# Kernel tuning notes

Measured on AMD Instinct MI355X. Metric: run time of the kernel, lower is better.

## Reference

```python
import jax, jax.numpy as jnp
import numpy as np

B, S, D = 2, 4096, 1024
H, HD = 16, 64
CF = 0.5
K = int(S * CF)          # top_k tokens routed through the block
HIDDEN = 4 * D
EPS = 1e-5
SCALE = 1.0 / float(np.sqrt(HD))


def rmsnorm(x, w):
    return x * jax.lax.rsqrt(jnp.mean(x * x, axis=-1, keepdims=True) + EPS) * w


def rope(x, cos, sin):
    # x: [B,K,H,HD]; cos/sin: [K, HD//2]
    x1, x2 = x[..., ::2], x[..., 1::2]
    c = cos[None, :, None, :]
    s = sin[None, :, None, :]
    r1 = x1 * c - x2 * s
    r2 = x1 * s + x2 * c
    return jnp.stack([r1, r2], axis=-1).reshape(x.shape)


def block(x, mask, cos, sin, attn_norm, wq, wk, wv, wo, ffn_norm, w1, w2, w3):
    # Llama-style decoder block on the routed subset x: [B,K,D]
    b, k, _ = x.shape
    xn = rmsnorm(x, attn_norm)
    q = (xn @ wq).reshape(b, k, H, HD)
    kk = (xn @ wk).reshape(b, k, H, HD)
    v = (xn @ wv).reshape(b, k, H, HD)
    q = rope(q, cos, sin)
    kk = rope(kk, cos, sin)
    scores = jnp.einsum('bqhd,bkhd->bhqk', q, kk) * SCALE
    scores = jnp.where(mask[None, None], scores, jnp.finfo(scores.dtype).min)
    attn = jax.nn.softmax(scores, axis=-1)
    o = jnp.einsum('bhqk,bkhd->bqhd', attn, v).reshape(b, k, D)
    h = x + o @ wo
    hn = rmsnorm(h, ffn_norm)
    return h + (jax.nn.silu(hn @ w1) * (hn @ w3)) @ w2


def setup_inputs() -> dict:
    key = jax.random.key(0)
    ks = jax.random.split(key, 10)
    sc = 0.02
    inv = 1.0 / (10000.0 ** (np.arange(0, HD, 2, dtype=np.float32) / HD))
    ang = np.outer(np.arange(K, dtype=np.float32), inv)  # [K, HD//2]
    return {
        'x': jax.random.normal(ks[0], (B, S, D), jnp.float32),
        'mask': jnp.tril(jnp.ones((K, K), dtype=bool)),
        'freqs_cos': jnp.asarray(np.cos(ang)),
        'freqs_sin': jnp.asarray(np.sin(ang)),
        'w_router': jax.random.normal(ks[1], (D, 1), jnp.float32) * sc,
        'attn_norm': jnp.ones((D,), jnp.float32),
        'wq': jax.random.normal(ks[2], (D, D), jnp.float32) * sc,
        'wk': jax.random.normal(ks[3], (D, D), jnp.float32) * sc,
        'wv': jax.random.normal(ks[4], (D, D), jnp.float32) * sc,
        'wo': jax.random.normal(ks[5], (D, D), jnp.float32) * sc,
        'ffn_norm': jnp.ones((D,), jnp.float32),
        'w1': jax.random.normal(ks[6], (D, HIDDEN), jnp.float32) * sc,
        'w2': jax.random.normal(ks[7], (HIDDEN, D), jnp.float32) * sc,
        'w3': jax.random.normal(ks[8], (D, HIDDEN), jnp.float32) * sc,
    }


def reference(x, mask, freqs_cos, freqs_sin, w_router, attn_norm, wq, wk, wv, wo, ffn_norm, w1, w2, w3):
    b = x.shape[0]
    router_logits = (x @ w_router)[..., 0]            # [B,S]
    vals, idx = jax.lax.top_k(router_logits, K)       # [B,K]
    order = jnp.argsort(idx, axis=1)                  # torch.sort of token_index
    sel = jnp.take_along_axis(idx, order, axis=1)     # sorted selected positions
    token_w = jax.nn.softmax(vals, axis=1)            # softmax over topk weights
    r_weights = jnp.take_along_axis(token_w, order, axis=1)  # [B,K]
    filtered_x = jnp.take_along_axis(x, sel[:, :, None], axis=1)  # [B,K,D]
    x_out = block(filtered_x, mask, freqs_cos, freqs_sin, attn_norm,
                  wq, wk, wv, wo, ffn_norm, w1, w2, w3)
    xw_out = r_weights[:, :, None] * x_out
    # scatter_add back into the residual stream
    out = x.at[jnp.arange(b)[:, None], sel, :].add(xw_out)
    return out
```

## Files before the change

kernel.cpp:

```cpp
#include <hip/hip_runtime.h>
#include <cstdint>
#include <cstddef>

typedef unsigned short u16;
typedef __bf16 bf16x8 __attribute__((ext_vector_type(8)));
typedef short s16x4 __attribute__((ext_vector_type(4)));
typedef float f32x4 __attribute__((ext_vector_type(4)));

#define SCALE_Q_LOG2E 0.18033688011112042f

static __device__ __forceinline__ float b2f(u16 u){ return __uint_as_float(((unsigned)u)<<16); }
static __device__ __forceinline__ u16 f2b(float f){
  unsigned u = __float_as_uint(f);
  return (u16)((u + 0x7fffu + ((u>>16)&1u)) >> 16);
}
static __device__ __forceinline__ void gload_lds16(const void* g, void* l){
  auto gp = reinterpret_cast<__attribute__((address_space(1))) uint32_t*>(reinterpret_cast<uintptr_t>(g));
  auto lp = reinterpret_cast<__attribute__((address_space(3))) uint32_t*>(reinterpret_cast<uintptr_t>(l));
  __builtin_amdgcn_global_load_lds(gp, lp, 16, 0, 0);
}
static __device__ __forceinline__ f32x4 mfma16bf(s16x4 a, s16x4 b, f32x4 c){
#if __has_builtin(__builtin_amdgcn_mfma_f32_16x16x16bf16_1k)
  return __builtin_amdgcn_mfma_f32_16x16x16bf16_1k(a, b, c, 0, 0, 0);
#else
  f32x4 d = c;
  asm volatile("v_mfma_f32_16x16x16_bf16 %0, %1, %2, %0" : "+v"(d) : "v"(a), "v"(b));
  return d;
#endif
}

__global__ __launch_bounds__(256) void transpose_f2b(const float* __restrict__ in, u16* __restrict__ out,
                                                     int R, int C, int rowmap){
  __shared__ float tile[32][33];
  int tx = threadIdx.x, ty = threadIdx.y;
  int c0 = blockIdx.x*32, r0 = blockIdx.y*32;
  #pragma unroll
  for (int i=0;i<4;i++) tile[ty+i*8][tx] = in[(size_t)(r0+ty+i*8)*C + c0+tx];
  __syncthreads();
  #pragma unroll
  for (int i=0;i<4;i++){
    int c = c0+ty+i*8;
    int orow = c;
    if (rowmap==1) orow = (c>>4)*32 + (c&15);
    else if (rowmap==2) orow = (c>>4)*32 + 16 + (c&15);
    out[(size_t)orow*R + r0+tx] = f2b(tile[tx][ty+i*8]);
  }
}

__global__ __launch_bounds__(256) void transpose_bf16(const u16* __restrict__ in, u16* __restrict__ out,
                                                      int R, int C){
  __shared__ u16 tile[32][33];
  size_t zoff = (size_t)blockIdx.z * R * C;
  const u16* ip = in + zoff;
  u16* op = out + zoff;
  int tx = threadIdx.x, ty = threadIdx.y;
  int c0 = blockIdx.x*32, r0 = blockIdx.y*32;
  #pragma unroll
  for (int i=0;i<4;i++) tile[ty+i*8][tx] = ip[(size_t)(r0+ty+i*8)*C + c0+tx];
  __syncthreads();
  #pragma unroll
  for (int i=0;i<4;i++) op[(size_t)(c0+ty+i*8)*R + r0+tx] = tile[tx][ty+i*8];
}

__global__ __launch_bounds__(256) void router_kernel(const float* __restrict__ x, const float* __restrict__ wr,
                                                     float* __restrict__ logits){
  int row = blockIdx.x*4 + (threadIdx.x>>6);
  int l = threadIdx.x & 63;
  const float4* xr = (const float4*)(x + (size_t)row*1024) + l;
  const float4* wp = (const float4*)wr + l;
  float acc = 0.f;
  #pragma unroll
  for (int c=0;c<4;c++){
    float4 xv = xr[c*64];
    float4 wv = wp[c*64];
    acc += xv.x*wv.x + xv.y*wv.y + xv.z*wv.z + xv.w*wv.w;
  }
  #pragma unroll
  for (int m=1;m<64;m<<=1) acc += __shfl_xor(acc, m, 64);
  if (l==0) logits[row] = acc;
}

static __device__ __forceinline__ unsigned mapkey(float f){
  unsigned u = __float_as_uint(f);
  return (u & 0x80000000u) ? ~u : (u | 0x80000000u);
}
static __device__ unsigned blk_scan_excl(unsigned cnt, unsigned* swav){
  int t = threadIdx.x; int l = t&63, w = t>>6;
  unsigned v = cnt;
  #pragma unroll
  for (int off=1; off<64; off<<=1){
    unsigned n = __shfl_up(v, off, 64);
    if (l >= off) v += n;
  }
  __syncthreads();
  if (l==63) swav[w] = v;
  __syncthreads();
  if (t==0){ unsigned c=0; for (int i=0;i<16;i++){ unsigned tmp=swav[i]; swav[i]=c; c+=tmp; } }
  __syncthreads();
  return swav[w] + v - cnt;
}
__global__ __launch_bounds__(1024) void topk_kernel(const float* __restrict__ logits,
        int* __restrict__ sel, float* __restrict__ rw, int* __restrict__ inv){
  int b = blockIdx.x, t = threadIdx.x;
  int l = t&63, w = t>>6;
  __shared__ float vals[4096];
  __shared__ unsigned hist[256];
  __shared__ unsigned swav[16];
  __shared__ float fwav[16];
  __shared__ unsigned sh_prefix, sh_remaining;
  const float* lgp = logits + b*4096;
  for (int i=t;i<4096;i+=1024) vals[i]=lgp[i];
  if (t==0){ sh_prefix=0u; sh_remaining=2048u; }
  __syncthreads();
  for (int level=0; level<4; level++){
    int shift = 24 - level*8;
    if (t<256) hist[t]=0u;
    __syncthreads();
    unsigned pfx = sh_prefix;
    for (int i=t;i<4096;i+=1024){
      unsigned key = mapkey(vals[i]);
      if (level==0 || (key >> (shift+8)) == pfx)
        atomicAdd(&hist[(key>>shift)&255u], 1u);
    }
    __syncthreads();
    if (t==0){
      unsigned rem = sh_remaining, cum=0u; unsigned bsel=0u;
      for (int bin=255; bin>=0; bin--){
        unsigned hc = hist[bin];
        if (cum + hc >= rem){ bsel=(unsigned)bin; break; }
        cum += hc;
      }
      sh_remaining = rem - cum;
      sh_prefix = (pfx<<8) | bsel;
    }
    __syncthreads();
  }
  unsigned T = sh_prefix;
  unsigned req = sh_remaining;
  int i0 = t*4;
  unsigned gt_[4], eq_[4], fl_[4]; float v_[4];
  #pragma unroll
  for (int j=0;j<4;j++){
    v_[j] = vals[i0+j];
    unsigned key = mapkey(v_[j]);
    gt_[j] = key > T ? 1u:0u;
    eq_[j] = key == T ? 1u:0u;
  }
  unsigned eqbase = blk_scan_excl(eq_[0]+eq_[1]+eq_[2]+eq_[3], swav);
  unsigned er = eqbase;
  #pragma unroll
  for (int j=0;j<4;j++){ fl_[j] = gt_[j] | (eq_[j] & (er < req ? 1u:0u)); er += eq_[j]; }
  unsigned pbase = blk_scan_excl(fl_[0]+fl_[1]+fl_[2]+fl_[3], swav);
  unsigned p = pbase;
  #pragma unroll
  for (int j=0;j<4;j++){
    int i = i0+j;
    if (fl_[j]){ sel[b*2048+(int)p]=i; inv[b*4096+i]=(int)p; p++; }
    else inv[b*4096+i] = -1;
  }
  float mx = fmaxf(fmaxf(v_[0],v_[1]), fmaxf(v_[2],v_[3]));
  #pragma unroll
  for (int m=1;m<64;m<<=1) mx = fmaxf(mx, __shfl_xor(mx,m,64));
  __syncthreads();
  if (l==0) fwav[w]=mx;
  __syncthreads();
  if (t==0){ float g=fwav[0]; for(int i=1;i<16;i++) g=fmaxf(g,fwav[i]); fwav[0]=g; }
  __syncthreads();
  float gm = fwav[0];
  float zz = 0.f;
  #pragma unroll
  for (int j=0;j<4;j++) if (fl_[j]) zz += expf(v_[j]-gm);
  #pragma unroll
  for (int m=1;m<64;m<<=1) zz += __shfl_xor(zz,m,64);
  __syncthreads();
  if (l==0) fwav[w]=zz;
  __syncthreads();
  if (t==0){ float s=0.f; for(int i=0;i<16;i++) s+=fwav[i]; fwav[0]=s; }
  __syncthreads();
  float Z = fwav[0];
  unsigned p2 = pbase;
  #pragma unroll
  for (int j=0;j<4;j++) if (fl_[j]){ rw[b*2048+(int)p2] = expf(v_[j]-gm)/Z; p2++; }
}

__global__ __launch_bounds__(256) void rmsnorm_kernel(const float* __restrict__ xin,
        const float* __restrict__ gamma, const int* __restrict__ sel,
        u16* __restrict__ xn){
  int r = blockIdx.x;
  int src = r;
  if (sel) src = (r>>11)*4096 + sel[r];
  const float* row = xin + (size_t)src*1024;
  int t = threadIdx.x, l = t&63, w = t>>6;
  int d0 = t*4;
  float4 xv = *(const float4*)(row + d0);
  float ss = xv.x*xv.x + xv.y*xv.y + xv.z*xv.z + xv.w*xv.w;
  #pragma unroll
  for (int m=1;m<64;m<<=1) ss += __shfl_xor(ss,m,64);
  __shared__ float red[4];
  if (l==0) red[w]=ss;
  __syncthreads();
  float tot = red[0]+red[1]+red[2]+red[3];
  float rms = rsqrtf(tot*(1.f/1024.f) + 1e-5f);
  float4 gv = *(const float4*)(gamma + d0);
  u16 o0=f2b(xv.x*rms*gv.x), o1=f2b(xv.y*rms*gv.y), o2=f2b(xv.z*rms*gv.z), o3=f2b(xv.w*rms*gv.w);
  uint2 ov; ov.x = (unsigned)o0 | ((unsigned)o1<<16); ov.y = (unsigned)o2 | ((unsigned)o3<<16);
  *(uint2*)(xn + (size_t)r*1024 + d0) = ov;
}

template<int BN, int BK, typename OT>
__global__ __launch_bounds__(256,2) void gemm_bt(const u16* __restrict__ A, const u16* __restrict__ Bt,
        OT* __restrict__ C, const float* __restrict__ resid, const int* __restrict__ sel,
        int M, int N, int Kd){
  __shared__ u16 As[128*BK];
  __shared__ u16 Bs[BN*BK];
  constexpr int NF = BN/32;
  constexpr int KK = BK/32;
  int t = threadIdx.x, w = t>>6, l = t&63, lg = l>>4, ln = l&15;
  int m0 = blockIdx.y*128, n0 = blockIdx.x*BN;
  int wm = (w&1)*64, wn = (w>>1)*(BN/2);
  f32x4 acc[4][NF] = {};
  for (int k0=0; k0<Kd; k0+=BK){
    __syncthreads();
    #pragma unroll
    for (int c=0;c<128*BK*2/4096;c++){
      int off = t*16 + c*4096;
      int row = off/(BK*2), ku = (off%(BK*2))>>1;
      gload_lds16(A + (size_t)(m0+row)*Kd + k0 + ku, &As[c*2048 + w*512]);
    }
    #pragma unroll
    for (int c=0;c<BN*BK*2/4096;c++){
      int off = t*16 + c*4096;
      int row = off/(BK*2), ku = (off%(BK*2))>>1;
      gload_lds16(Bt + (size_t)(n0+row)*Kd + k0 + ku, &Bs[c*2048 + w*512]);
    }
    __syncthreads();
    #pragma unroll
    for (int kk=0;kk<KK;kk++){
      bf16x8 af[4], bfv[NF];
      #pragma unroll
      for (int i=0;i<4;i++)  af[i]  = *(const bf16x8*)&As[(wm+i*16+ln)*BK + kk*32 + lg*8];
      #pragma unroll
      for (int i=0;i<NF;i++) bfv[i] = *(const bf16x8*)&Bs[(wn+i*16+ln)*BK + kk*32 + lg*8];
      #pragma unroll
      for (int mi=0;mi<4;mi++)
        #pragma unroll
        for (int ni=0;ni<NF;ni++)
          acc[mi][ni] = __builtin_amdgcn_mfma_f32_16x16x32_bf16(af[mi], bfv[ni], acc[mi][ni], 0,0,0);
    }
  }
  #pragma unroll
  for (int mi=0;mi<4;mi++){
    #pragma unroll
    for (int ni=0;ni<NF;ni++){
      #pragma unroll
      for (int r=0;r<4;r++){
        int row = m0+wm+mi*16+lg*4+r;
        int col = n0+wn+ni*16+ln;
        float v = acc[mi][ni][r];
        if (resid){
          size_t rrow = sel ? ((size_t)(row>>11)*4096 + sel[row]) : (size_t)row;
          v += resid[rrow*N + col];
        }
        if constexpr (sizeof(OT)==2) C[(size_t)row*N + col] = f2b(v);
        else                          C[(size_t)row*N + col] = v;
      }
    }
  }
}

__global__ __launch_bounds__(256,2) void gemm13(const u16* __restrict__ A, const u16* __restrict__ Bt,
        u16* __restrict__ g, int Kd){
  __shared__ u16 As[128*32];
  __shared__ u16 Bs[128*32];
  int t = threadIdx.x, w = t>>6, l = t&63, lg = l>>4, ln = l&15;
  int m0 = blockIdx.y*128, n0 = blockIdx.x*128;
  int wm = (w&1)*64, wn = (w>>1)*64;
  f32x4 acc[4][4] = {};
  for (int k0=0; k0<Kd; k0+=32){
    __syncthreads();
    #pragma unroll
    for (int c=0;c<2;c++){
      int off = t*16 + c*4096;
      int row = off>>6, ku = (off&63)>>1;
      gload_lds16(A  + (size_t)(m0+row)*Kd + k0 + ku, &As[c*2048 + w*512]);
      gload_lds16(Bt + (size_t)(n0+row)*Kd + k0 + ku, &Bs[c*2048 + w*512]);
    }
    __syncthreads();
    bf16x8 af[4], bfv[4];
    #pragma unroll
    for (int i=0;i<4;i++){
      af[i]  = *(const bf16x8*)&As[(wm+i*16+ln)*32 + lg*8];
      bfv[i] = *(const bf16x8*)&Bs[(wn+i*16+ln)*32 + lg*8];
    }
    #pragma unroll
    for (int mi=0;mi<4;mi++)
      #pragma unroll
      for (int ni=0;ni<4;ni++)
        acc[mi][ni] = __builtin_amdgcn_mfma_f32_16x16x32_bf16(af[mi], bfv[ni], acc[mi][ni], 0,0,0);
  }
  int gbase = (n0+wn)>>1;
  #pragma unroll
  for (int mi=0;mi<4;mi++){
    #pragma unroll
    for (int p=0;p<2;p++){
      #pragma unroll
      for (int r=0;r<4;r++){
        int row = m0+wm+mi*16+lg*4+r;
        int col = gbase + p*16 + ln;
        float a1 = acc[mi][2*p][r], a3 = acc[mi][2*p+1][r];
        float s1 = a1 / (1.f + __expf(-a1));
        g[(size_t)row*4096 + col] = f2b(s1*a3);
      }
    }
  }
}

__global__ __launch_bounds__(256) void rope_kernel(const u16* __restrict__ QKV,
        const float* __restrict__ fcos, const float* __restrict__ fsin,
        u16* __restrict__ q_r, u16* __restrict__ k_r, u16* __restrict__ v_r){
  int row = blockIdx.x;
  int tok = row & 2047;
  int t = threadIdx.x;
  int d0 = t*4;
  int h = d0 >> 6, wd = d0 & 63, i0 = wd >> 1;
  const u16* base = QKV + (size_t)row*3072;
  size_t ob = (((size_t)(row>>11)*16 + h)*2048 + (size_t)tok)*64 + wd;
  float c0 = fcos[tok*32+i0],   s0 = fsin[tok*32+i0];
  float c1 = fcos[tok*32+i0+1], s1 = fsin[tok*32+i0+1];
  const u16* qp = base + d0;
  float x0=b2f(qp[0]), x1=b2f(qp[1]), x2=b2f(qp[2]), x3=b2f(qp[3]);
  q_r[ob]   = f2b((x0*c0-x1*s0)*SCALE_Q_LOG2E);
  q_r[ob+1] = f2b((x0*s0+x1*c0)*SCALE_Q_LOG2E);
  q_r[ob+2] = f2b((x2*c1-x3*s1)*SCALE_Q_LOG2E);
  q_r[ob+3] = f2b((x2*s1+x3*c1)*SCALE_Q_LOG2E);
  const u16* kp = base + 1024 + d0;
  x0=b2f(kp[0]); x1=b2f(kp[1]); x2=b2f(kp[2]); x3=b2f(kp[3]);
  k_r[ob]   = f2b(x0*c0-x1*s0);
  k_r[ob+1] = f2b(x0*s0+x1*c0);
  k_r[ob+2] = f2b(x2*c1-x3*s1);
  k_r[ob+3] = f2b(x2*s1+x3*c1);
  const u16* vp = base + 2048 + d0;
  v_r[ob]=vp[0]; v_r[ob+1]=vp[1]; v_r[ob+2]=vp[2]; v_r[ob+3]=vp[3];
}

__global__ __launch_bounds__(256,2) void flash_kernel(const u16* __restrict__ q_r,
        const u16* __restrict__ k_r, const u16* __restrict__ v_t, u16* __restrict__ o){
  const int S = 2048;
  int pr = blockIdx.x, bh = blockIdx.y;
  int b = bh>>4, h = bh&15;
  int t = threadIdx.x, w = t>>6, l = t&63, lg = l>>4, ln = l&15;
  __shared__ u16 Ks[2][64*72];
  __shared__ u16 Vs[2][64*72];
  const u16* qb = q_r + (size_t)bh*S*64;
  const u16* kb = k_r + (size_t)bh*S*64;
  const u16* vb = v_t + (size_t)bh*64*S;
  int rr = t>>2, p16 = (t&3)*16;
  #pragma unroll
  for (int ti=0; ti<2; ti++){
    int qt = ti ? (31-pr) : pr;
    int q0 = qt*64;
    int q = q0 + w*16 + ln;
    bf16x8 qf0 = *(const bf16x8*)(qb + (size_t)q*64 + lg*8);
    bf16x8 qf1 = *(const bf16x8*)(qb + (size_t)q*64 + 32 + lg*8);
    f32x4 oaccT[4] = {};
    float mi = -1e30f, li = 0.f;
    __syncthreads();
    {
      *(bf16x8*)&Ks[0][rr*72+p16]   = *(const bf16x8*)(kb + (size_t)rr*64 + p16);
      *(bf16x8*)&Ks[0][rr*72+p16+8] = *(const bf16x8*)(kb + (size_t)rr*64 + p16 + 8);
      *(bf16x8*)&Vs[0][rr*72+p16]   = *(const bf16x8*)(vb + (size_t)rr*S + p16);
      *(bf16x8*)&Vs[0][rr*72+p16+8] = *(const bf16x8*)(vb + (size_t)rr*S + p16 + 8);
    }
    __syncthreads();
    for (int kv=0; kv<=qt; kv++){
      int cur = kv&1;
      int k0 = kv*64;
      bool hasnext = kv < qt;
      bf16x8 nk0, nk1, nv0, nv1;
      if (hasnext){
        int kn = k0 + 64;
        nk0 = *(const bf16x8*)(kb + (size_t)(kn+rr)*64 + p16);
        nk1 = *(const bf16x8*)(kb + (size_t)(kn+rr)*64 + p16 + 8);
        nv0 = *(const bf16x8*)(vb + (size_t)rr*S + kn + p16);
        nv1 = *(const bf16x8*)(vb + (size_t)rr*S + kn + p16 + 8);
      }
      f32x4 sv[4];
      #pragma unroll
      for (int ni=0;ni<4;ni++){
        bf16x8 kf0 = *(const bf16x8*)&Ks[cur][(ni*16+ln)*72 + lg*8];
        bf16x8 kf1 = *(const bf16x8*)&Ks[cur][(ni*16+ln)*72 + 32 + lg*8];
        f32x4 z = {};
        z = __builtin_amdgcn_mfma_f32_16x16x32_bf16(kf0, qf0, z, 0,0,0);
        z = __builtin_amdgcn_mfma_f32_16x16x32_bf16(kf1, qf1, z, 0,0,0);
        sv[ni] = z;
      }
      bool diag = (kv==qt);
      float rm = -1e30f;
      if (diag){
        #pragma unroll
        for (int ni=0;ni<4;ni++)
          #pragma unroll
          for (int r=0;r<4;r++){
            float xs = sv[ni][r];
            if (k0+ni*16+lg*4+r > q) xs = -1e30f;
            sv[ni][r] = xs;
            rm = fmaxf(rm, xs);
          }
      } else {
        #pragma unroll
        for (int ni=0;ni<4;ni++)
          #pragma unroll
          for (int r=0;r<4;r++) rm = fmaxf(rm, sv[ni][r]);
      }
      rm = fmaxf(rm, __shfl_xor(rm, 16, 64));
      rm = fmaxf(rm, __shfl_xor(rm, 32, 64));
      float mn = fmaxf(mi, rm);
      float alpha = exp2f(mi - mn);
      float ls = 0.f;
      s16x4 pf[4];
      #pragma unroll
      for (int ni=0;ni<4;ni++){
        float p0 = exp2f(sv[ni][0]-mn);
        float p1 = exp2f(sv[ni][1]-mn);
        float p2 = exp2f(sv[ni][2]-mn);
        float p3 = exp2f(sv[ni][3]-mn);
        ls += (p0+p1)+(p2+p3);
        s16x4 pp;
        pp[0]=(short)f2b(p0); pp[1]=(short)f2b(p1); pp[2]=(short)f2b(p2); pp[3]=(short)f2b(p3);
        pf[ni]=pp;
      }
      ls += __shfl_xor(ls, 16, 64);
      ls += __shfl_xor(ls, 32, 64);
      li = li*alpha + ls;
      mi = mn;
      #pragma unroll
      for (int dt=0; dt<4; dt++){
        f32x4 oo = oaccT[dt];
        oo[0]*=alpha; oo[1]*=alpha; oo[2]*=alpha; oo[3]*=alpha;
        #pragma unroll
        for (int ni=0;ni<4;ni++){
          s16x4 vf = *(const s16x4*)&Vs[cur][(dt*16+ln)*72 + ni*16 + lg*4];
          oo = mfma16bf(vf, pf[ni], oo);
        }
        oaccT[dt] = oo;
      }
      if (hasnext){
        int nb = cur^1;
        *(bf16x8*)&Ks[nb][rr*72+p16]   = nk0;
        *(bf16x8*)&Ks[nb][rr*72+p16+8] = nk1;
        *(bf16x8*)&Vs[nb][rr*72+p16]   = nv0;
        *(bf16x8*)&Vs[nb][rr*72+p16+8] = nv1;
      }
      __syncthreads();
    }
    {
      int tok = q0 + w*16 + ln;
      u16* ob = o + ((size_t)(b*S+tok))*1024 + h*64 + lg*4;
      #pragma unroll
      for (int dt=0; dt<4; dt++){
        u16 a0=f2b(oaccT[dt][0]/li), a1=f2b(oaccT[dt][1]/li);
        u16 a2=f2b(oaccT[dt][2]/li), a3=f2b(oaccT[dt][3]/li);
        uint2 pv; pv.x = (unsigned)a0 | ((unsigned)a1<<16); pv.y = (unsigned)a2 | ((unsigned)a3<<16);
        *(uint2*)(ob + dt*16) = pv;
      }
    }
  }
}

__global__ __launch_bounds__(256) void final_kernel(const float* __restrict__ x, const float* __restrict__ h,
        const u16* __restrict__ y, const int* __restrict__ inv, const float* __restrict__ rw,
        float* __restrict__ out){
  int row = blockIdx.x;
  int b = row>>12;
  int t = threadIdx.x, d0 = t*4;
  float4 xv = *(const float4*)(x + (size_t)row*1024 + d0);
  float4* op = (float4*)(out + (size_t)row*1024 + d0);
  int j = inv[row];
  if (j < 0){ *op = xv; return; }
  int fr = b*2048 + j;
  float wgt = rw[fr];
  float4 hv = *(const float4*)(h + (size_t)fr*1024 + d0);
  uint2 yv = *(const uint2*)(y + (size_t)fr*1024 + d0);
  float y0=b2f((u16)(yv.x&0xffffu)), y1=b2f((u16)(yv.x>>16)), y2=b2f((u16)(yv.y&0xffffu)), y3=b2f((u16)(yv.y>>16));
  float4 ov;
  ov.x = xv.x + wgt*(hv.x + y0);
  ov.y = xv.y + wgt*(hv.y + y1);
  ov.z = xv.z + wgt*(hv.z + y2);
  ov.w = xv.w + wgt*(hv.w + y3);
  *op = ov;
}

extern "C" void kernel_launch(void* const* d_in, const int* in_sizes, int n_in,
                              void* d_out, int out_size, void* d_ws, size_t ws_size,
                              hipStream_t stream) {
  (void)in_sizes; (void)n_in; (void)out_size; (void)ws_size;
  const float* x     = (const float*)d_in[0];
  const float* fcos  = (const float*)d_in[2];
  const float* fsin  = (const float*)d_in[3];
  const float* wr    = (const float*)d_in[4];
  const float* anorm = (const float*)d_in[5];
  const float* wq    = (const float*)d_in[6];
  const float* wk    = (const float*)d_in[7];
  const float* wv    = (const float*)d_in[8];
  const float* wo    = (const float*)d_in[9];
  const float* fnorm = (const float*)d_in[10];
  const float* w1    = (const float*)d_in[11];
  const float* w2    = (const float*)d_in[12];
  const float* w3    = (const float*)d_in[13];
  float* out = (float*)d_out;

  char* W = (char*)d_ws;
  const size_t MB = 1024*1024;
  u16* WqkvT = (u16*)(W + 0);
  u16* WoT   = (u16*)(W + 6*MB);
  u16* W13T  = (u16*)(W + 8*MB);
  u16* W2T   = (u16*)(W + 24*MB);
  u16* xn    = (u16*)(W + 32*MB);
  u16* QKV   = (u16*)(W + 40*MB);
  u16* q_r   = (u16*)(W + 64*MB);
  u16* k_r   = (u16*)(W + 72*MB);
  u16* v_r   = (u16*)(W + 80*MB);
  u16* v_t   = (u16*)(W + 88*MB);
  u16* attno = (u16*)(W + 96*MB);
  float* hbuf= (float*)(W + 104*MB);
  u16* hn    = (u16*)(W + 120*MB);
  u16* g     = (u16*)(W + 128*MB);
  u16* ybuf  = (u16*)(W + 32*MB);
  float* logits = (float*)(W + 160*MB);
  int*   sel    = (int*)(W + 160*MB + 64*1024);
  float* rw     = (float*)(W + 160*MB + 96*1024);
  int*   inv    = (int*)(W + 160*MB + 128*1024);

  dim3 tb(32,8);
  transpose_f2b<<<dim3(32,32,1),  tb, 0, stream>>>(wq, WqkvT,                1024, 1024, 0);
  transpose_f2b<<<dim3(32,32,1),  tb, 0, stream>>>(wk, WqkvT + 1024*1024,    1024, 1024, 0);
  transpose_f2b<<<dim3(32,32,1),  tb, 0, stream>>>(wv, WqkvT + 2*1024*1024,  1024, 1024, 0);
  transpose_f2b<<<dim3(32,32,1),  tb, 0, stream>>>(wo, WoT,                  1024, 1024, 0);
  transpose_f2b<<<dim3(128,32,1), tb, 0, stream>>>(w1, W13T,                 1024, 4096, 1);
  transpose_f2b<<<dim3(128,32,1), tb, 0, stream>>>(w3, W13T,                 1024, 4096, 2);
  transpose_f2b<<<dim3(32,128,1), tb, 0, stream>>>(w2, W2T,                  4096, 1024, 0);

  router_kernel<<<2048, 256, 0, stream>>>(x, wr, logits);
  topk_kernel<<<2, 1024, 0, stream>>>(logits, sel, rw, inv);
  rmsnorm_kernel<<<4096, 256, 0, stream>>>(x, anorm, sel, xn);
  gemm_bt<128,32,u16><<<dim3(24,32), 256, 0, stream>>>(xn, WqkvT, QKV, nullptr, nullptr, 4096, 3072, 1024);
  rope_kernel<<<4096, 256, 0, stream>>>(QKV, fcos, fsin, q_r, k_r, v_r);
  transpose_bf16<<<dim3(2,64,32), tb, 0, stream>>>(v_r, v_t, 2048, 64);
  flash_kernel<<<dim3(16,32), 256, 0, stream>>>(q_r, k_r, v_t, attno);
  gemm_bt<64,32,float><<<dim3(16,32), 256, 0, stream>>>(attno, WoT, hbuf, x, sel, 4096, 1024, 1024);
  rmsnorm_kernel<<<4096, 256, 0, stream>>>(hbuf, fnorm, nullptr, hn);
  gemm13<<<dim3(64,32), 256, 0, stream>>>(hn, W13T, g, 1024);
  gemm_bt<64,64,u16><<<dim3(16,32), 256, 0, stream>>>(g, W2T, ybuf, nullptr, nullptr, 4096, 1024, 4096);
  final_kernel<<<8192, 256, 0, stream>>>(x, hbuf, ybuf, inv, rw, out);
}
```

Before: 526.5 us.

## Swizzle GEMM LDS tiles, deepen K tiles, fuse weight prep, share KV across query tiles

Merges the seven weight transpose launches into one prep_weights kernel. Adds an XOR swizzle to the GEMM LDS layout to cut bank conflicts, and raises the K tile to 64 for the QKV, Wo and W1/W3 GEMMs so each barrier covers more MFMAs. The flash kernel now handles its two query tiles (low and high) in a single pass over K/V, so shared tiles are loaded once and used by both. This adds register pressure (two accumulator sets) and more LDS per block, which may lower occupancy.

```diff
diff --git a/kernel.cpp b/kernel.cpp
--- a/kernel.cpp
+++ b/kernel.cpp
@@ -29,11 +29,32 @@
 #endif
 }
 
-__global__ __launch_bounds__(256) void transpose_f2b(const float* __restrict__ in, u16* __restrict__ out,
-                                                     int R, int C, int rowmap){
+__global__ __launch_bounds__(256) void prep_weights(
+    const float* __restrict__ wq, const float* __restrict__ wk,
+    const float* __restrict__ wv, const float* __restrict__ wo,
+    const float* __restrict__ w1, const float* __restrict__ w3,
+    const float* __restrict__ w2,
+    u16* __restrict__ WqkvT, u16* __restrict__ WoT,
+    u16* __restrict__ W13T, u16* __restrict__ W2T){
   __shared__ float tile[32][33];
-  int tx = threadIdx.x, ty = threadIdx.y;
-  int c0 = blockIdx.x*32, r0 = blockIdx.y*32;
+  int bx = blockIdx.x;
+  const float* in; u16* out; int R, C, rowmap, tcol, trow;
+  if (bx < 4096){
+    int wsel = bx>>10, tid = bx&1023;
+    in = (wsel==0)?wq:(wsel==1)?wk:(wsel==2)?wv:wo;
+    out = (wsel<3) ? (WqkvT + (size_t)wsel*1024*1024) : WoT;
+    R=1024; C=1024; rowmap=0; tcol=tid&31; trow=tid>>5;
+  } else if (bx < 12288){
+    int wsel=(bx-4096)>>12, tid=(bx-4096)&4095;
+    in = wsel ? w3 : w1; out = W13T; R=1024; C=4096; rowmap=1+wsel;
+    tcol=tid&127; trow=tid>>7;
+  } else {
+    int tid = bx-12288;
+    in = w2; out = W2T; R=4096; C=1024; rowmap=0;
+    tcol=tid&31; trow=tid>>5;
+  }
+  int t=threadIdx.x, tx=t&31, ty=t>>5;
+  int c0=tcol*32, r0=trow*32;
   #pragma unroll
   for (int i=0;i<4;i++) tile[ty+i*8][tx] = in[(size_t)(r0+ty+i*8)*C + c0+tx];
   __syncthreads();
@@ -205,6 +226,12 @@
   u16 o0=f2b(xv.x*rms*gv.x), o1=f2b(xv.y*rms*gv.y), o2=f2b(xv.z*rms*gv.z), o3=f2b(xv.w*rms*gv.w);
   uint2 ov; ov.x = (unsigned)o0 | ((unsigned)o1<<16); ov.y = (unsigned)o2 | ((unsigned)o3<<16);
   *(uint2*)(xn + (size_t)r*1024 + d0) = ov;
+}
+
+template<int BK>
+static __device__ __forceinline__ int swz(int row, int blk){
+  if constexpr (BK==64) return blk ^ (row&7);
+  else                  return blk ^ ((row>>1)&3);
 }
 
 template<int BN, int BK, typename OT>
@@ -224,23 +251,29 @@
     #pragma unroll
     for (int c=0;c<128*BK*2/4096;c++){
       int off = t*16 + c*4096;
-      int row = off/(BK*2), ku = (off%(BK*2))>>1;
-      gload_lds16(A + (size_t)(m0+row)*Kd + k0 + ku, &As[c*2048 + w*512]);
+      int row = off/(BK*2), pb = (off%(BK*2))>>4;
+      gload_lds16(A + (size_t)(m0+row)*Kd + k0 + swz<BK>(row,pb)*8, &As[c*2048 + w*512]);
     }
     #pragma unroll
     for (int c=0;c<BN*BK*2/4096;c++){
       int off = t*16 + c*4096;
-      int row = off/(BK*2), ku = (off%(BK*2))>>1;
-      gload_lds16(Bt + (size_t)(n0+row)*Kd + k0 + ku, &Bs[c*2048 + w*512]);
+      int row = off/(BK*2), pb = (off%(BK*2))>>4;
+      gload_lds16(Bt + (size_t)(n0+row)*Kd + k0 + swz<BK>(row,pb)*8, &Bs[c*2048 + w*512]);
     }
     __syncthreads();
     #pragma unroll
     for (int kk=0;kk<KK;kk++){
       bf16x8 af[4], bfv[NF];
       #pragma unroll
-      for (int i=0;i<4;i++)  af[i]  = *(const bf16x8*)&As[(wm+i*16+ln)*BK + kk*32 + lg*8];
-      #pragma unroll
-      for (int i=0;i<NF;i++) bfv[i] = *(const bf16x8*)&Bs[(wn+i*16+ln)*BK + kk*32 + lg*8];
+      for (int i=0;i<4;i++){
+        int r = wm+i*16+ln;
+        af[i] = *(const bf16x8*)&As[r*BK + swz<BK>(r, kk*4+lg)*8];
+      }
+      #pragma unroll
+      for (int i=0;i<NF;i++){
+        int r = wn+i*16+ln;
+        bfv[i] = *(const bf16x8*)&Bs[r*BK + swz<BK>(r, kk*4+lg)*8];
+      }
       #pragma unroll
       for (int mi=0;mi<4;mi++)
         #pragma unroll
@@ -270,33 +303,38 @@
 
 __global__ __launch_bounds__(256,2) void gemm13(const u16* __restrict__ A, const u16* __restrict__ Bt,
         u16* __restrict__ g, int Kd){
-  __shared__ u16 As[128*32];
-  __shared__ u16 Bs[128*32];
+  constexpr int BK = 64;
+  __shared__ u16 As[128*BK];
+  __shared__ u16 Bs[128*BK];
   int t = threadIdx.x, w = t>>6, l = t&63, lg = l>>4, ln = l&15;
   int m0 = blockIdx.y*128, n0 = blockIdx.x*128;
   int wm = (w&1)*64, wn = (w>>1)*64;
   f32x4 acc[4][4] = {};
-  for (int k0=0; k0<Kd; k0+=32){
-    __syncthreads();
-    #pragma unroll
-    for (int c=0;c<2;c++){
+  for (int k0=0; k0<Kd; k0+=BK){
+    __syncthreads();
+    #pragma unroll
+    for (int c=0;c<4;c++){
       int off = t*16 + c*4096;
-      int row = off>>6, ku = (off&63)>>1;
-      gload_lds16(A  + (size_t)(m0+row)*Kd + k0 + ku, &As[c*2048 + w*512]);
-      gload_lds16(Bt + (size_t)(n0+row)*Kd + k0 + ku, &Bs[c*2048 + w*512]);
-    }
-    __syncthreads();
-    bf16x8 af[4], bfv[4];
-    #pragma unroll
-    for (int i=0;i<4;i++){
-      af[i]  = *(const bf16x8*)&As[(wm+i*16+ln)*32 + lg*8];
-      bfv[i] = *(const bf16x8*)&Bs[(wn+i*16+ln)*32 + lg*8];
-    }
-    #pragma unroll
-    for (int mi=0;mi<4;mi++)
-      #pragma unroll
-      for (int ni=0;ni<4;ni++)
-        acc[mi][ni] = __builtin_amdgcn_mfma_f32_16x16x32_bf16(af[mi], bfv[ni], acc[mi][ni], 0,0,0);
+      int row = off/(BK*2), pb = (off%(BK*2))>>4;
+      gload_lds16(A  + (size_t)(m0+row)*Kd + k0 + swz<BK>(row,pb)*8, &As[c*2048 + w*512]);
+      gload_lds16(Bt + (size_t)(n0+row)*Kd + k0 + swz<BK>(row,pb)*8, &Bs[c*2048 + w*512]);
+    }
+    __syncthreads();
+    #pragma unroll
+    for (int kk=0;kk<2;kk++){
+      bf16x8 af[4], bfv[4];
+      #pragma unroll
+      for (int i=0;i<4;i++){
+        int ra = wm+i*16+ln, rb = wn+i*16+ln;
+        af[i]  = *(const bf16x8*)&As[ra*BK + swz<BK>(ra, kk*4+lg)*8];
+        bfv[i] = *(const bf16x8*)&Bs[rb*BK + swz<BK>(rb, kk*4+lg)*8];
+      }
+      #pragma unroll
+      for (int mi=0;mi<4;mi++)
+        #pragma unroll
+        for (int ni=0;ni<4;ni++)
+          acc[mi][ni] = __builtin_amdgcn_mfma_f32_16x16x32_bf16(af[mi], bfv[ni], acc[mi][ni], 0,0,0);
+    }
   }
   int gbase = (n0+wn)>>1;
   #pragma unroll
@@ -343,6 +381,71 @@
   v_r[ob]=vp[0]; v_r[ob+1]=vp[1]; v_r[ob+2]=vp[2]; v_r[ob+3]=vp[3];
 }
 
+static __device__ __forceinline__ void flash_tile(
+    const u16* __restrict__ Ksb, const u16* __restrict__ Vsb,
+    bf16x8 qf0, bf16x8 qf1, int k0, int q, bool diag,
+    int lg, int ln, float& mi, float& li, f32x4* oaccT){
+  f32x4 sv[4];
+  #pragma unroll
+  for (int ni=0;ni<4;ni++){
+    bf16x8 kf0 = *(const bf16x8*)&Ksb[(ni*16+ln)*72 + lg*8];
+    bf16x8 kf1 = *(const bf16x8*)&Ksb[(ni*16+ln)*72 + 32 + lg*8];
+    f32x4 z = {};
+    z = __builtin_amdgcn_mfma_f32_16x16x32_bf16(kf0, qf0, z, 0,0,0);
+    z = __builtin_amdgcn_mfma_f32_16x16x32_bf16(kf1, qf1, z, 0,0,0);
+    sv[ni] = z;
+  }
+  float rm = -1e30f;
+  if (diag){
+    #pragma unroll
+    for (int ni=0;ni<4;ni++)
+      #pragma unroll
+      for (int r=0;r<4;r++){
+        float xs = sv[ni][r];
+        if (k0+ni*16+lg*4+r > q) xs = -1e30f;
+        sv[ni][r] = xs;
+        rm = fmaxf(rm, xs);
+      }
+  } else {
+    #pragma unroll
+    for (int ni=0;ni<4;ni++)
+      #pragma unroll
+      for (int r=0;r<4;r++) rm = fmaxf(rm, sv[ni][r]);
+  }
+  rm = fmaxf(rm, __shfl_xor(rm, 16, 64));
+  rm = fmaxf(rm, __shfl_xor(rm, 32, 64));
+  float mn = fmaxf(mi, rm);
+  float alpha = exp2f(mi - mn);
+  float ls = 0.f;
+  s16x4 pf[4];
+  #pragma unroll
+  for (int ni=0;ni<4;ni++){
+    float p0 = exp2f(sv[ni][0]-mn);
+    float p1 = exp2f(sv[ni][1]-mn);
+    float p2 = exp2f(sv[ni][2]-mn);
+    float p3 = exp2f(sv[ni][3]-mn);
+    ls += (p0+p1)+(p2+p3);
+    s16x4 pp;
+    pp[0]=(short)f2b(p0); pp[1]=(short)f2b(p1); pp[2]=(short)f2b(p2); pp[3]=(short)f2b(p3);
+    pf[ni]=pp;
+  }
+  ls += __shfl_xor(ls, 16, 64);
+  ls += __shfl_xor(ls, 32, 64);
+  li = li*alpha + ls;
+  mi = mn;
+  #pragma unroll
+  for (int dt=0; dt<4; dt++){
+    f32x4 oo = oaccT[dt];
+    oo[0]*=alpha; oo[1]*=alpha; oo[2]*=alpha; oo[3]*=alpha;
+    #pragma unroll
+    for (int ni=0;ni<4;ni++){
+      s16x4 vf = *(const s16x4*)&Vsb[(dt*16+ln)*72 + ni*16 + lg*4];
+      oo = mfma16bf(vf, pf[ni], oo);
+    }
+    oaccT[dt] = oo;
+  }
+}
+
 __global__ __launch_bounds__(256,2) void flash_kernel(const u16* __restrict__ q_r,
         const u16* __restrict__ k_r, const u16* __restrict__ v_t, u16* __restrict__ o){
   const int S = 2048;
@@ -355,114 +458,64 @@
   const u16* kb = k_r + (size_t)bh*S*64;
   const u16* vb = v_t + (size_t)bh*64*S;
   int rr = t>>2, p16 = (t&3)*16;
-  #pragma unroll
-  for (int ti=0; ti<2; ti++){
-    int qt = ti ? (31-pr) : pr;
-    int q0 = qt*64;
-    int q = q0 + w*16 + ln;
-    bf16x8 qf0 = *(const bf16x8*)(qb + (size_t)q*64 + lg*8);
-    bf16x8 qf1 = *(const bf16x8*)(qb + (size_t)q*64 + 32 + lg*8);
-    f32x4 oaccT[4] = {};
-    float mi = -1e30f, li = 0.f;
-    __syncthreads();
-    {
-      *(bf16x8*)&Ks[0][rr*72+p16]   = *(const bf16x8*)(kb + (size_t)rr*64 + p16);
-      *(bf16x8*)&Ks[0][rr*72+p16+8] = *(const bf16x8*)(kb + (size_t)rr*64 + p16 + 8);
-      *(bf16x8*)&Vs[0][rr*72+p16]   = *(const bf16x8*)(vb + (size_t)rr*S + p16);
-      *(bf16x8*)&Vs[0][rr*72+p16+8] = *(const bf16x8*)(vb + (size_t)rr*S + p16 + 8);
-    }
-    __syncthreads();
-    for (int kv=0; kv<=qt; kv++){
-      int cur = kv&1;
-      int k0 = kv*64;
-      bool hasnext = kv < qt;
-      bf16x8 nk0, nk1, nv0, nv1;
-      if (hasnext){
-        int kn = k0 + 64;
-        nk0 = *(const bf16x8*)(kb + (size_t)(kn+rr)*64 + p16);
-        nk1 = *(const bf16x8*)(kb + (size_t)(kn+rr)*64 + p16 + 8);
-        nv0 = *(const bf16x8*)(vb + (size_t)rr*S + kn + p16);
-        nv1 = *(const bf16x8*)(vb + (size_t)rr*S + kn + p16 + 8);
-      }
-      f32x4 sv[4];
-      #pragma unroll
-      for (int ni=0;ni<4;ni++){
-        bf16x8 kf0 = *(const bf16x8*)&Ks[cur][(ni*16+ln)*72 + lg*8];
-        bf16x8 kf1 = *(const bf16x8*)&Ks[cur][(ni*16+ln)*72 + 32 + lg*8];
-        f32x4 z = {};
-        z = __builtin_amdgcn_mfma_f32_16x16x32_bf16(kf0, qf0, z, 0,0,0);
-        z = __builtin_amdgcn_mfma_f32_16x16x32_bf16(kf1, qf1, z, 0,0,0);
-        sv[ni] = z;
-      }
-      bool diag = (kv==qt);
-      float rm = -1e30f;
-      if (diag){
-        #pragma unroll
-        for (int ni=0;ni<4;ni++)
-          #pragma unroll
-          for (int r=0;r<4;r++){
-            float xs = sv[ni][r];
-            if (k0+ni*16+lg*4+r > q) xs = -1e30f;
-            sv[ni][r] = xs;
-            rm = fmaxf(rm, xs);
-          }
-      } else {
-        #pragma unroll
-        for (int ni=0;ni<4;ni++)
-          #pragma unroll
-          for (int r=0;r<4;r++) rm = fmaxf(rm, sv[ni][r]);
-      }
-      rm = fmaxf(rm, __shfl_xor(rm, 16, 64));
-      rm = fmaxf(rm, __shfl_xor(rm, 32, 64));
-      float mn = fmaxf(mi, rm);
-      float alpha = exp2f(mi - mn);
-      float ls = 0.f;
-      s16x4 pf[4];
-      #pragma unroll
-      for (int ni=0;ni<4;ni++){
-        float p0 = exp2f(sv[ni][0]-mn);
-        float p1 = exp2f(sv[ni][1]-mn);
-        float p2 = exp2f(sv[ni][2]-mn);
-        float p3 = exp2f(sv[ni][3]-mn);
-        ls += (p0+p1)+(p2+p3);
-        s16x4 pp;
-        pp[0]=(short)f2b(p0); pp[1]=(short)f2b(p1); pp[2]=(short)f2b(p2); pp[3]=(short)f2b(p3);
-        pf[ni]=pp;
-      }
-      ls += __shfl_xor(ls, 16, 64);
-      ls += __shfl_xor(ls, 32, 64);
-      li = li*alpha + ls;
-      mi = mn;
-      #pragma unroll
-      for (int dt=0; dt<4; dt++){
-        f32x4 oo = oaccT[dt];
-        oo[0]*=alpha; oo[1]*=alpha; oo[2]*=alpha; oo[3]*=alpha;
-        #pragma unroll
-        for (int ni=0;ni<4;ni++){
-          s16x4 vf = *(const s16x4*)&Vs[cur][(dt*16+ln)*72 + ni*16 + lg*4];
-          oo = mfma16bf(vf, pf[ni], oo);
-        }
-        oaccT[dt] = oo;
-      }
-      if (hasnext){
-        int nb = cur^1;
-        *(bf16x8*)&Ks[nb][rr*72+p16]   = nk0;
-        *(bf16x8*)&Ks[nb][rr*72+p16+8] = nk1;
-        *(bf16x8*)&Vs[nb][rr*72+p16]   = nv0;
-        *(bf16x8*)&Vs[nb][rr*72+p16+8] = nv1;
-      }
-      __syncthreads();
-    }
-    {
-      int tok = q0 + w*16 + ln;
-      u16* ob = o + ((size_t)(b*S+tok))*1024 + h*64 + lg*4;
-      #pragma unroll
-      for (int dt=0; dt<4; dt++){
-        u16 a0=f2b(oaccT[dt][0]/li), a1=f2b(oaccT[dt][1]/li);
-        u16 a2=f2b(oaccT[dt][2]/li), a3=f2b(oaccT[dt][3]/li);
-        uint2 pv; pv.x = (unsigned)a0 | ((unsigned)a1<<16); pv.y = (unsigned)a2 | ((unsigned)a3<<16);
-        *(uint2*)(ob + dt*16) = pv;
-      }
+  int qlo = pr, qhi = 31-pr;
+  int qAr = qlo*64 + w*16 + ln;
+  int qBr = qhi*64 + w*16 + ln;
+  bf16x8 qA0 = *(const bf16x8*)(qb + (size_t)qAr*64 + lg*8);
+  bf16x8 qA1 = *(const bf16x8*)(qb + (size_t)qAr*64 + 32 + lg*8);
+  bf16x8 qB0 = *(const bf16x8*)(qb + (size_t)qBr*64 + lg*8);
+  bf16x8 qB1 = *(const bf16x8*)(qb + (size_t)qBr*64 + 32 + lg*8);
+  f32x4 oA[4] = {}, oB[4] = {};
+  float miA=-1e30f, liA=0.f, miB=-1e30f, liB=0.f;
+  {
+    *(bf16x8*)&Ks[0][rr*72+p16]   = *(const bf16x8*)(kb + (size_t)rr*64 + p16);
+    *(bf16x8*)&Ks[0][rr*72+p16+8] = *(const bf16x8*)(kb + (size_t)rr*64 + p16 + 8);
+    *(bf16x8*)&Vs[0][rr*72+p16]   = *(const bf16x8*)(vb + (size_t)rr*S + p16);
+    *(bf16x8*)&Vs[0][rr*72+p16+8] = *(const bf16x8*)(vb + (size_t)rr*S + p16 + 8);
+  }
+  __syncthreads();
+  for (int kv=0; kv<=qhi; kv++){
+    int cur = kv&1;
+    int k0 = kv*64;
+    bool hasnext = kv < qhi;
+    bf16x8 nk0, nk1, nv0, nv1;
+    if (hasnext){
+      int kn = k0 + 64;
+      nk0 = *(const bf16x8*)(kb + (size_t)(kn+rr)*64 + p16);
+      nk1 = *(const bf16x8*)(kb + (size_t)(kn+rr)*64 + p16 + 8);
+      nv0 = *(const bf16x8*)(vb + (size_t)rr*S + kn + p16);
+      nv1 = *(const bf16x8*)(vb + (size_t)rr*S + kn + p16 + 8);
+    }
+    if (kv <= qlo)
+      flash_tile(Ks[cur], Vs[cur], qA0, qA1, k0, qAr, kv==qlo, lg, ln, miA, liA, oA);
+    flash_tile(Ks[cur], Vs[cur], qB0, qB1, k0, qBr, kv==qhi, lg, ln, miB, liB, oB);
+    if (hasnext){
+      int nb = cur^1;
+      *(bf16x8*)&Ks[nb][rr*72+p16]   = nk0;
+      *(bf16x8*)&Ks[nb][rr*72+p16+8] = nk1;
+      *(bf16x8*)&Vs[nb][rr*72+p16]   = nv0;
+      *(bf16x8*)&Vs[nb][rr*72+p16+8] = nv1;
+    }
+    __syncthreads();
+  }
+  {
+    u16* ob = o + ((size_t)(b*S+qAr))*1024 + h*64 + lg*4;
+    #pragma unroll
+    for (int dt=0; dt<4; dt++){
+      u16 a0=f2b(oA[dt][0]/liA), a1=f2b(oA[dt][1]/liA);
+      u16 a2=f2b(oA[dt][2]/liA), a3=f2b(oA[dt][3]/liA);
+      uint2 pv; pv.x = (unsigned)a0 | ((unsigned)a1<<16); pv.y = (unsigned)a2 | ((unsigned)a3<<16);
+      *(uint2*)(ob + dt*16) = pv;
+    }
+  }
+  {
+    u16* ob = o + ((size_t)(b*S+qBr))*1024 + h*64 + lg*4;
+    #pragma unroll
+    for (int dt=0; dt<4; dt++){
+      u16 a0=f2b(oB[dt][0]/liB), a1=f2b(oB[dt][1]/liB);
+      u16 a2=f2b(oB[dt][2]/liB), a3=f2b(oB[dt][3]/liB);
+      uint2 pv; pv.x = (unsigned)a0 | ((unsigned)a1<<16); pv.y = (unsigned)a2 | ((unsigned)a3<<16);
+      *(uint2*)(ob + dt*16) = pv;
     }
   }
 }
@@ -531,23 +584,15 @@
   float* rw     = (float*)(W + 160*MB + 96*1024);
   int*   inv    = (int*)(W + 160*MB + 128*1024);
 
-  dim3 tb(32,8);
-  transpose_f2b<<<dim3(32,32,1),  tb, 0, stream>>>(wq, WqkvT,                1024, 1024, 0);
-  transpose_f2b<<<dim3(32,32,1),  tb, 0, stream>>>(wk, WqkvT + 1024*1024,    1024, 1024, 0);
-  transpose_f2b<<<dim3(32,32,1),  tb, 0, stream>>>(wv, WqkvT + 2*1024*1024,  1024, 1024, 0);
-  transpose_f2b<<<dim3(32,32,1),  tb, 0, stream>>>(wo, WoT,                  1024, 1024, 0);
-  transpose_f2b<<<dim3(128,32,1), tb, 0, stream>>>(w1, W13T,                 1024, 4096, 1);
-  transpose_f2b<<<dim3(128,32,1), tb, 0, stream>>>(w3, W13T,                 1024, 4096, 2);
-  transpose_f2b<<<dim3(32,128,1), tb, 0, stream>>>(w2, W2T,                  4096, 1024, 0);
-
+  prep_weights<<<16384, 256, 0, stream>>>(wq, wk, wv, wo, w1, w3, w2, WqkvT, WoT, W13T, W2T);
   router_kernel<<<2048, 256, 0, stream>>>(x, wr, logits);
   topk_kernel<<<2, 1024, 0, stream>>>(logits, sel, rw, inv);
   rmsnorm_kernel<<<4096, 256, 0, stream>>>(x, anorm, sel, xn);
-  gemm_bt<128,32,u16><<<dim3(24,32), 256, 0, stream>>>(xn, WqkvT, QKV, nullptr, nullptr, 4096, 3072, 1024);
+  gemm_bt<128,64,u16><<<dim3(24,32), 256, 0, stream>>>(xn, WqkvT, QKV, nullptr, nullptr, 4096, 3072, 1024);
   rope_kernel<<<4096, 256, 0, stream>>>(QKV, fcos, fsin, q_r, k_r, v_r);
-  transpose_bf16<<<dim3(2,64,32), tb, 0, stream>>>(v_r, v_t, 2048, 64);
+  transpose_bf16<<<dim3(2,64,32), dim3(32,8), 0, stream>>>(v_r, v_t, 2048, 64);
   flash_kernel<<<dim3(16,32), 256, 0, stream>>>(q_r, k_r, v_t, attno);
-  gemm_bt<64,32,float><<<dim3(16,32), 256, 0, stream>>>(attno, WoT, hbuf, x, sel, 4096, 1024, 1024);
+  gemm_bt<64,64,float><<<dim3(16,32), 256, 0, stream>>>(attno, WoT, hbuf, x, sel, 4096, 1024, 1024);
   rmsnorm_kernel<<<4096, 256, 0, stream>>>(hbuf, fnorm, nullptr, hn);
   gemm13<<<dim3(64,32), 256, 0, stream>>>(hn, W13T, g, 1024);
   gemm_bt<64,64,u16><<<dim3(16,32), 256, 0, stream>>>(g, W2T, ybuf, nullptr, nullptr, 4096, 1024, 4096);
```

Measured after the change: 489.4 us. -7.0%, faster.
